# Performance work log

Hardware: AMD Instinct MI355X
Metric: run time of the kernel (lower is better)

Reference implementation:

```python
import jax, jax.numpy as jnp
import numpy as np

B, M, Q, D = 32, 8192, 64, 128

def setup_inputs() -> dict:
    key = jax.random.key(0)
    k1, k2, k3, k4 = jax.random.split(key, 4)
    story_a = jax.random.normal(k1, (B, M, D), dtype=jnp.float32)
    u = jax.random.normal(k2, (B, Q, D), dtype=jnp.float32)
    story_c = jax.random.normal(k3, (B, M, D), dtype=jnp.float32)
    H = jax.random.normal(k4, (D, D), dtype=jnp.float32) * (1.0 / np.sqrt(D))
    return {"story_a": story_a, "u": u, "story_c": story_c, "H": H}

def reference(story_a, u, story_c, H):
    # scores: Dot(axes=-1)([story_a, u]) -> (B, M, Q)
    m = jnp.einsum('bmd,bqd->bmq', story_a, u)
    # Keras Softmax() default axis=-1: normalize over Q (faithful to original)
    p = jax.nn.softmax(m, axis=-1)          # (B, M, Q)
    p = jnp.swapaxes(p, 1, 2)                # (B, Q, M)
    # output memory: Dot(axes=(2,1))([p, story_c]) -> (B, Q, D)
    c = jnp.einsum('bqm,bmd->bqd', p, story_c)
    # linear residual: K.dot(u, H) + c
    mapped_u = jnp.einsum('bqd,de->bqe', u, H)
    return c + mapped_u
```

## Files before the change

### kernel.cpp

```cpp
#include <hip/hip_runtime.h>

#define B_ 32
#define M_ 8192
#define Q_ 64
#define D_ 128
#define MT 64
#define LDA 136
#define LDP 72

typedef __attribute__((ext_vector_type(8))) short short8;
typedef __attribute__((ext_vector_type(4))) float floatx4;

__device__ __forceinline__ unsigned short f2bf(float x) {
  union { float f; unsigned u; } t; t.f = x;
  unsigned r = t.u + 0x7fffu + ((t.u >> 16) & 1u);
  return (unsigned short)(r >> 16);
}

__global__ __launch_bounds__(256, 2) void memn2n_main(
    const float* __restrict__ A, const float* __restrict__ U,
    const float* __restrict__ Cc, float* __restrict__ dst,
    int chunks, int use_atomic) {
  __shared__ __align__(16) unsigned short sU[Q_ * LDA];
  __shared__ __align__(16) unsigned short sA[MT * LDA];
  __shared__ __align__(16) unsigned short sC[MT * LDA];
  __shared__ __align__(16) unsigned short sP[Q_ * LDP];

  const int tid  = threadIdx.x;
  const int lane = tid & 63;
  const int w    = tid >> 6;
  const int l15  = lane & 15;
  const int quad = (lane >> 4) & 3;

  const int blk = blockIdx.x;
  const int b   = blk / chunks;
  const int ch  = blk - b * chunks;
  const int Mc  = M_ / chunks;
  const int m0  = ch * Mc;

  const int g = tid & 31;
  const int r = tid >> 5;

  const float* ub = U + (size_t)b * Q_ * D_;
#pragma unroll
  for (int i = 0; i < 8; ++i) {
    int row = r + 8 * i;
    float4 v = *(const float4*)(ub + row * D_ + 4 * g);
    ushort4 h = make_ushort4(f2bf(v.x), f2bf(v.y), f2bf(v.z), f2bf(v.w));
    *(ushort4*)&sU[row * LDA + 4 * g] = h;
  }

  floatx4 acc[2][4];
#pragma unroll
  for (int i = 0; i < 2; ++i)
#pragma unroll
    for (int j = 0; j < 4; ++j) acc[i][j] = (floatx4){0.f, 0.f, 0.f, 0.f};

  const float* Abase = A + (size_t)b * M_ * D_ + (size_t)m0 * D_;
  const float* Cbase = Cc + (size_t)b * M_ * D_ + (size_t)m0 * D_;

  const int nT = Mc / MT;
  for (int t = 0; t < nT; ++t) {
    __syncthreads();
    const float* At = Abase + (size_t)t * MT * D_;
    const float* Ct = Cbase + (size_t)t * MT * D_;
#pragma unroll
    for (int i = 0; i < 8; ++i) {
      int mi = r + 8 * i;
      float4 va = *(const float4*)(At + mi * D_ + 4 * g);
      float4 vc = *(const float4*)(Ct + mi * D_ + 4 * g);
      ushort4 ha = make_ushort4(f2bf(va.x), f2bf(va.y), f2bf(va.z), f2bf(va.w));
      ushort4 hc = make_ushort4(f2bf(vc.x), f2bf(vc.y), f2bf(vc.z), f2bf(vc.w));
      *(ushort4*)&sA[mi * LDA + 4 * g] = ha;
      *(ushort4*)&sC[mi * LDA + 4 * g] = hc;
    }
    __syncthreads();

    floatx4 s1[4];
#pragma unroll
    for (int qs = 0; qs < 4; ++qs) s1[qs] = (floatx4){0.f, 0.f, 0.f, 0.f};
#pragma unroll
    for (int ks = 0; ks < 4; ++ks) {
      short8 af = *(const short8*)&sA[(16 * w + l15) * LDA + 32 * ks + 8 * quad];
#pragma unroll
      for (int qs = 0; qs < 4; ++qs) {
        short8 bfv = *(const short8*)&sU[(16 * qs + l15) * LDA + 32 * ks + 8 * quad];
        s1[qs] = __builtin_amdgcn_mfma_f32_16x16x32_bf16(af, bfv, s1[qs], 0, 0, 0);
      }
    }

    float pv[4][4];
#pragma unroll
    for (int rg = 0; rg < 4; ++rg) {
      float v0 = s1[0][rg], v1 = s1[1][rg], v2 = s1[2][rg], v3 = s1[3][rg];
      float mx = fmaxf(fmaxf(v0, v1), fmaxf(v2, v3));
#pragma unroll
      for (int m = 1; m <= 8; m <<= 1) mx = fmaxf(mx, __shfl_xor(mx, m, 64));
      const float c = 1.4426950408889634f;
      float e0 = exp2f((v0 - mx) * c), e1 = exp2f((v1 - mx) * c);
      float e2 = exp2f((v2 - mx) * c), e3 = exp2f((v3 - mx) * c);
      float sm = e0 + e1 + e2 + e3;
#pragma unroll
      for (int m = 1; m <= 8; m <<= 1) sm += __shfl_xor(sm, m, 64);
      float inv = 1.0f / sm;
      pv[0][rg] = e0 * inv; pv[1][rg] = e1 * inv;
      pv[2][rg] = e2 * inv; pv[3][rg] = e3 * inv;
    }
#pragma unroll
    for (int qs = 0; qs < 4; ++qs) {
      ushort4 h = make_ushort4(f2bf(pv[qs][0]), f2bf(pv[qs][1]),
                               f2bf(pv[qs][2]), f2bf(pv[qs][3]));
      *(ushort4*)&sP[(16 * qs + l15) * LDP + 16 * w + 4 * quad] = h;
    }
    __syncthreads();

#pragma unroll
    for (int ks = 0; ks < 2; ++ks) {
      short8 pa[4];
#pragma unroll
      for (int qs = 0; qs < 4; ++qs)
        pa[qs] = *(const short8*)&sP[(16 * qs + l15) * LDP + 32 * ks + 8 * quad];
#pragma unroll
      for (int ds = 0; ds < 2; ++ds) {
        int d = l15 + 16 * (2 * w + ds);
        union { unsigned short u[8]; short8 v; } bb;
#pragma unroll
        for (int j = 0; j < 8; ++j)
          bb.u[j] = sC[(32 * ks + 8 * quad + j) * LDA + d];
#pragma unroll
        for (int qs = 0; qs < 4; ++qs)
          acc[ds][qs] = __builtin_amdgcn_mfma_f32_16x16x32_bf16(pa[qs], bb.v, acc[ds][qs], 0, 0, 0);
      }
    }
  }

  if (use_atomic) {
#pragma unroll
    for (int ds = 0; ds < 2; ++ds)
#pragma unroll
      for (int qs = 0; qs < 4; ++qs)
#pragma unroll
        for (int rg = 0; rg < 4; ++rg) {
          int q = qs * 16 + quad * 4 + rg;
          int d = l15 + 16 * (2 * w + ds);
          atomicAdd(&dst[((size_t)b * Q_ + q) * D_ + d], acc[ds][qs][rg]);
        }
  } else {
    float* pp = dst + (((size_t)ch * B_ + b) * Q_) * D_;
#pragma unroll
    for (int ds = 0; ds < 2; ++ds)
#pragma unroll
      for (int qs = 0; qs < 4; ++qs)
#pragma unroll
        for (int rg = 0; rg < 4; ++rg) {
          int q = qs * 16 + quad * 4 + rg;
          int d = l15 + 16 * (2 * w + ds);
          pp[q * D_ + d] = acc[ds][qs][rg];
        }
  }
}

__global__ __launch_bounds__(128) void memn2n_reduce(
    const float* __restrict__ U, const float* __restrict__ H,
    const float* __restrict__ part, float* __restrict__ out, int chunks) {
  int bq = blockIdx.x;
  int b = bq >> 6, q = bq & 63;
  int d = threadIdx.x;
  __shared__ float su[D_];
  size_t row = ((size_t)b * Q_ + q) * D_;
  su[d] = U[row + d];
  __syncthreads();
  float acc = 0.f;
#pragma unroll 16
  for (int e = 0; e < D_; ++e) acc = fmaf(su[e], H[e * D_ + d], acc);
  for (int ch = 0; ch < chunks; ++ch)
    acc += part[(((size_t)ch * B_ + b) * Q_ + q) * D_ + d];
  out[row + d] = acc;
}

extern "C" void kernel_launch(void* const* d_in, const int* in_sizes, int n_in,
                              void* d_out, int out_size, void* d_ws, size_t ws_size,
                              hipStream_t stream) {
  const float* A  = (const float*)d_in[0];
  const float* U  = (const float*)d_in[1];
  const float* Cc = (const float*)d_in[2];
  const float* H  = (const float*)d_in[3];
  float* out = (float*)d_out;

  const int CH = 16;
  size_t need = (size_t)CH * B_ * Q_ * D_ * sizeof(float);
  if (ws_size >= need) {
    float* part = (float*)d_ws;
    memn2n_main<<<B_ * CH, 256, 0, stream>>>(A, U, Cc, part, CH, 0);
    memn2n_reduce<<<B_ * Q_, 128, 0, stream>>>(U, H, part, out, CH);
  } else {
    memn2n_reduce<<<B_ * Q_, 128, 0, stream>>>(U, H, nullptr, out, 0);
    memn2n_main<<<B_ * 8, 256, 0, stream>>>(A, U, Cc, out, 8, 1);
  }
}
```

Baseline: 300.9 us.

## Prefetch next A/C tile into registers and keep U fragments in registers

Global loads for the next 64-row A and C tile are issued right after the tile is written to shared memory, so they overlap with the MFMA and softmax work of the current tile. The U operand is converted to bf16 fragments once and held in registers instead of being re-read from LDS on every tile, which also removes the sU buffer. The barrier after the P write is replaced by an inline-asm waitcnt plus s_barrier. The register-held fragments and 64 floats of prefetch per thread raise register pressure, which may spill or lower occupancy under the 2-blocks launch bound.

```diff
diff --git a/kernel.cpp b/kernel.cpp
--- a/kernel.cpp
+++ b/kernel.cpp
@@ -5,6 +5,7 @@
 #define Q_ 64
 #define D_ 128
 #define MT 64
+#define CH 16
 #define LDA 136
 #define LDP 72
 
@@ -17,11 +18,21 @@
   return (unsigned short)(r >> 16);
 }
 
+__device__ __forceinline__ short8 pack8(float4 a, float4 b) {
+  union { unsigned short u[8]; short8 v; } o;
+  o.u[0] = f2bf(a.x); o.u[1] = f2bf(a.y); o.u[2] = f2bf(a.z); o.u[3] = f2bf(a.w);
+  o.u[4] = f2bf(b.x); o.u[5] = f2bf(b.y); o.u[6] = f2bf(b.z); o.u[7] = f2bf(b.w);
+  return o.v;
+}
+
+__device__ __forceinline__ void barrier_lds() {
+  asm volatile("s_waitcnt lgkmcnt(0)\n\ts_barrier" ::: "memory");
+}
+
 __global__ __launch_bounds__(256, 2) void memn2n_main(
     const float* __restrict__ A, const float* __restrict__ U,
     const float* __restrict__ Cc, float* __restrict__ dst,
     int chunks, int use_atomic) {
-  __shared__ __align__(16) unsigned short sU[Q_ * LDA];
   __shared__ __align__(16) unsigned short sA[MT * LDA];
   __shared__ __align__(16) unsigned short sC[MT * LDA];
   __shared__ __align__(16) unsigned short sP[Q_ * LDP];
@@ -42,13 +53,16 @@
   const int r = tid >> 5;
 
   const float* ub = U + (size_t)b * Q_ * D_;
-#pragma unroll
-  for (int i = 0; i < 8; ++i) {
-    int row = r + 8 * i;
-    float4 v = *(const float4*)(ub + row * D_ + 4 * g);
-    ushort4 h = make_ushort4(f2bf(v.x), f2bf(v.y), f2bf(v.z), f2bf(v.w));
-    *(ushort4*)&sU[row * LDA + 4 * g] = h;
-  }
+  short8 uf[4][4];
+#pragma unroll
+  for (int qs = 0; qs < 4; ++qs)
+#pragma unroll
+    for (int ks = 0; ks < 4; ++ks) {
+      const float* p = ub + (16 * qs + l15) * D_ + 32 * ks + 8 * quad;
+      float4 x = *(const float4*)p;
+      float4 y = *(const float4*)(p + 4);
+      uf[qs][ks] = pack8(x, y);
+    }
 
   floatx4 acc[2][4];
 #pragma unroll
@@ -60,22 +74,38 @@
   const float* Cbase = Cc + (size_t)b * M_ * D_ + (size_t)m0 * D_;
 
   const int nT = Mc / MT;
+
+  float4 pA[8], pC[8];
+#pragma unroll
+  for (int i = 0; i < 8; ++i) {
+    int mi = r + 8 * i;
+    pA[i] = *(const float4*)(Abase + mi * D_ + 4 * g);
+    pC[i] = *(const float4*)(Cbase + mi * D_ + 4 * g);
+  }
+
   for (int t = 0; t < nT; ++t) {
     __syncthreads();
-    const float* At = Abase + (size_t)t * MT * D_;
-    const float* Ct = Cbase + (size_t)t * MT * D_;
 #pragma unroll
     for (int i = 0; i < 8; ++i) {
       int mi = r + 8 * i;
-      float4 va = *(const float4*)(At + mi * D_ + 4 * g);
-      float4 vc = *(const float4*)(Ct + mi * D_ + 4 * g);
-      ushort4 ha = make_ushort4(f2bf(va.x), f2bf(va.y), f2bf(va.z), f2bf(va.w));
-      ushort4 hc = make_ushort4(f2bf(vc.x), f2bf(vc.y), f2bf(vc.z), f2bf(vc.w));
+      ushort4 ha = make_ushort4(f2bf(pA[i].x), f2bf(pA[i].y), f2bf(pA[i].z), f2bf(pA[i].w));
+      ushort4 hc = make_ushort4(f2bf(pC[i].x), f2bf(pC[i].y), f2bf(pC[i].z), f2bf(pC[i].w));
       *(ushort4*)&sA[mi * LDA + 4 * g] = ha;
       *(ushort4*)&sC[mi * LDA + 4 * g] = hc;
     }
     __syncthreads();
 
+    if (t + 1 < nT) {
+      const float* An = Abase + (size_t)(t + 1) * MT * D_;
+      const float* Cn = Cbase + (size_t)(t + 1) * MT * D_;
+#pragma unroll
+      for (int i = 0; i < 8; ++i) {
+        int mi = r + 8 * i;
+        pA[i] = *(const float4*)(An + mi * D_ + 4 * g);
+        pC[i] = *(const float4*)(Cn + mi * D_ + 4 * g);
+      }
+    }
+
     floatx4 s1[4];
 #pragma unroll
     for (int qs = 0; qs < 4; ++qs) s1[qs] = (floatx4){0.f, 0.f, 0.f, 0.f};
@@ -83,10 +113,8 @@
     for (int ks = 0; ks < 4; ++ks) {
       short8 af = *(const short8*)&sA[(16 * w + l15) * LDA + 32 * ks + 8 * quad];
 #pragma unroll
-      for (int qs = 0; qs < 4; ++qs) {
-        short8 bfv = *(const short8*)&sU[(16 * qs + l15) * LDA + 32 * ks + 8 * quad];
-        s1[qs] = __builtin_amdgcn_mfma_f32_16x16x32_bf16(af, bfv, s1[qs], 0, 0, 0);
-      }
+      for (int qs = 0; qs < 4; ++qs)
+        s1[qs] = __builtin_amdgcn_mfma_f32_16x16x32_bf16(af, uf[qs][ks], s1[qs], 0, 0, 0);
     }
 
     float pv[4][4];
@@ -112,7 +140,7 @@
                                f2bf(pv[qs][2]), f2bf(pv[qs][3]));
       *(ushort4*)&sP[(16 * qs + l15) * LDP + 16 * w + 4 * quad] = h;
     }
-    __syncthreads();
+    barrier_lds();
 
 #pragma unroll
     for (int ks = 0; ks < 2; ++ks) {
@@ -187,7 +215,6 @@
   const float* H  = (const float*)d_in[3];
   float* out = (float*)d_out;
 
-  const int CH = 16;
   size_t need = (size_t)CH * B_ * Q_ * D_ * sizeof(float);
   if (ws_size >= need) {
     float* part = (float*)d_ws;
```

Result: no change. 304.7 us (+1.3%).
